# Optimization experiments

Measured on AMD Instinct MI355X. Metric: run time of the kernel, lower is better.

Reference implementation:

```python
import jax, jax.numpy as jnp
import numpy as np

N_NODES = 30000
N_EDGES = 480000
NODE_DIM = 16
NUM_RADIAL = 8
NUM_ELEMENTS = 120
R_MAX = 5.0
NUM_BLOCKS = 2
N_PATHS = 5  # h0*sh0->0e, h0*sh1->1o, h0*sh2->2e, h1.sh1->0e, h2.sh2->0e


def _sh_basis(u):
    # real spherical harmonics up to l=2, component normalization, on unit vectors u [E,3]
    x, y, z = u[:, 0], u[:, 1], u[:, 2]
    s15 = jnp.sqrt(jnp.asarray(15.0, u.dtype))
    s5 = jnp.sqrt(jnp.asarray(5.0, u.dtype))
    sh1 = jnp.sqrt(jnp.asarray(3.0, u.dtype)) * u                      # [E,3]
    sh2 = jnp.stack([s15 * x * y, s15 * y * z,
                     0.5 * s5 * (3.0 * z * z - 1.0),
                     s15 * x * z, 0.5 * s15 * (x * x - y * y)], -1)    # [E,5]
    return sh1, sh2


def _energy(pos, emb, W_init, Wr, br, W_out, W_read, W1, b1, W2, b2, z, edge_index):
    N = pos.shape[0]
    row, col = edge_index[0], edge_index[1]
    edge_vec = pos[row] - pos[col]                                     # [E,3] gather
    r = jnp.sqrt(jnp.sum(edge_vec * edge_vec, -1) + 1e-12)             # [E]
    n = jnp.arange(1, NUM_RADIAL + 1, dtype=pos.dtype)
    # Bessel radial basis: sqrt(2/rc) * sin(n*pi*r/rc)/r
    radial = jnp.sqrt(2.0 / R_MAX) * jnp.sin(n[None, :] * jnp.pi * r[:, None] / R_MAX) / r[:, None]  # [E,R]
    u = edge_vec / r[:, None]
    sh1, sh2 = _sh_basis(u)

    # initial projection: embedding scalars -> 0e channels; l=1,l=2 start at zero
    h0 = emb[z] @ W_init                                               # [N,C]
    h1 = jnp.zeros((N, NODE_DIM, 3), pos.dtype)
    h2 = jnp.zeros((N, NODE_DIM, 5), pos.dtype)

    for b in range(NUM_BLOCKS):
        w = (radial @ Wr[b] + br[b]).reshape(-1, N_PATHS, NODE_DIM)    # [E,P,C] radial path weights
        h0c, h1c, h2c = h0[col], h1[col], h2[col]
        # scalar messages: h0*sh0 + <h1,sh1> + <h2,sh2>
        m0 = (w[:, 0] * h0c
              + w[:, 3] * jnp.einsum('ecm,em->ec', h1c, sh1)
              + w[:, 4] * jnp.einsum('ecm,em->ec', h2c, sh2))          # [E,C]
        m1 = (w[:, 1] * h0c)[:, :, None] * sh1[:, None, :]             # [E,C,3]
        m2 = (w[:, 2] * h0c)[:, :, None] * sh2[:, None, :]             # [E,C,5]
        a0 = jax.ops.segment_sum(m0, row, num_segments=N)
        a1 = jax.ops.segment_sum(m1, row, num_segments=N)
        a2 = jax.ops.segment_sum(m2, row, num_segments=N)
        h0 = h0 + a0 @ W_out[b, 0]
        h1 = h1 + jnp.einsum('ncm,cd->ndm', a1, W_out[b, 1])
        h2 = h2 + jnp.einsum('ncm,cd->ndm', a2, W_out[b, 2])

    inv = h0 @ W_read                                                  # readout 0e part
    site = jax.nn.silu(inv @ W1 + b1) @ W2 + b2                        # [N,1]
    return jnp.sum(site)


def setup_inputs() -> dict:
    key = jax.random.key(0)
    ks = jax.random.split(key, 12)
    C, R = NODE_DIM, NUM_RADIAL
    s = 1.0 / np.sqrt(C)
    return {
        'pos': jax.random.normal(ks[0], (N_NODES, 3), jnp.float32) * 3.0,
        'z': jax.random.randint(ks[1], (N_NODES,), 0, NUM_ELEMENTS),
        'edge_index': jax.random.randint(ks[2], (2, N_EDGES), 0, N_NODES),
        'emb': jax.random.normal(ks[3], (NUM_ELEMENTS, C), jnp.float32),
        'W_init': jax.random.normal(ks[4], (C, C), jnp.float32) * s,
        'Wr': jax.random.normal(ks[5], (NUM_BLOCKS, R, N_PATHS * C), jnp.float32) / np.sqrt(R),
        'br': jnp.zeros((NUM_BLOCKS, N_PATHS * C), jnp.float32),
        'W_out': jax.random.normal(ks[6], (NUM_BLOCKS, 3, C, C), jnp.float32) * s,
        'W_read': jax.random.normal(ks[7], (C, C), jnp.float32) * s,
        'W1': jax.random.normal(ks[8], (C, C), jnp.float32) * s,
        'b1': jnp.zeros((C,), jnp.float32),
        'W2': jax.random.normal(ks[9], (C, 1), jnp.float32) * s,
        'b2': jnp.zeros((1,), jnp.float32),
    }


def reference(pos, z, edge_index, emb, W_init, Wr, br, W_out, W_read, W1, b1, W2, b2):
    e_fn = lambda p: _energy(p, emb, W_init, Wr, br, W_out, W_read, W1, b1, W2, b2, z, edge_index)
    total, dE_dpos = jax.value_and_grad(e_fn)(pos)
    energy = jnp.reshape(total, (1, 1))
    forces = -dE_dpos
    return energy, forces
```

## Files before the change

kernel.cpp:

```cpp
#include <hip/hip_runtime.h>
#include <math.h>

#ifndef M_PI
#define M_PI 3.14159265358979323846
#endif

static inline int cdiv(int a, int b){ return (a + b - 1) / b; }

#define SQRT3f  1.7320508075688772f
#define SQRT5f  2.23606797749979f
#define SQRT15f 3.872983346207417f
#define KRADf   0.6324555320336759f
#define PI5f    0.6283185307179586f
#define KPI5f   (KRADf * PI5f)


__device__ __forceinline__ float grp16_sum(float v){
  v += __shfl_xor(v, 1, 64);
  v += __shfl_xor(v, 2, 64);
  v += __shfl_xor(v, 4, 64);
  v += __shfl_xor(v, 8, 64);
  return v;
}
__device__ __forceinline__ float xgrp_sum(float v){
  v += __shfl_xor(v, 16, 64);
  v += __shfl_xor(v, 32, 64);
  return v;
}

__device__ __forceinline__ void sh_from_u(float ux, float uy, float uz,
                                          float* sh1, float* sh2)
{
  sh1[0] = SQRT3f*ux; sh1[1] = SQRT3f*uy; sh1[2] = SQRT3f*uz;
  sh2[0] = SQRT15f*ux*uy;
  sh2[1] = SQRT15f*uy*uz;
  sh2[2] = 0.5f*SQRT5f*(3.f*uz*uz - 1.f);
  sh2[3] = SQRT15f*ux*uz;
  sh2[4] = 0.5f*SQRT15f*(ux*ux - uy*uy);
}


__global__ void k_hist(const int* __restrict__ ei, int E,
                       int* __restrict__ deg_row, int* __restrict__ deg_col)
{
  int e = blockIdx.x * blockDim.x + threadIdx.x;
  if (e >= E) return;
  atomicAdd(&deg_row[ei[e]], 1);
  atomicAdd(&deg_col[ei[E + e]], 1);
}

__global__ void k_alloc(const int* __restrict__ deg_row, const int* __restrict__ deg_col,
                        int* __restrict__ start_row, int* __restrict__ cur_row,
                        int* __restrict__ start_col, int* __restrict__ cur_col,
                        int* __restrict__ cursors, int N)
{
  int idx = blockIdx.x * blockDim.x + threadIdx.x;
  int lane = threadIdx.x & 63;
  #pragma unroll
  for (int which = 0; which < 2; which++) {
    const int* deg = which ? deg_col : deg_row;
    int* start = which ? start_col : start_row;
    int* cur   = which ? cur_col   : cur_row;
    int v = (idx < N) ? deg[idx] : 0;
    int incl = v;
    #pragma unroll
    for (int d = 1; d < 64; d <<= 1) {
      int y = __shfl_up(incl, d, 64);
      if (lane >= d) incl += y;
    }
    int wtot = __shfl(incl, 63, 64);
    int base = 0;
    if (lane == 63) base = atomicAdd(&cursors[which], wtot);
    base = __shfl(base, 63, 64);
    if (idx < N) { int st = base + incl - v; start[idx] = st; cur[idx] = st; }
  }
}

__global__ void k_scatter_geom(const float* __restrict__ pos, const int* __restrict__ ei, int E,
                               int* __restrict__ cur_row, int* __restrict__ cur_col,
                               float4* __restrict__ uR, float2* __restrict__ scR,
                               float4* __restrict__ uC, float2* __restrict__ scC,
                               int* __restrict__ colR, int* __restrict__ cposR,
                               int* __restrict__ rowC, int* __restrict__ rposC)
{
  int e = blockIdx.x * blockDim.x + threadIdx.x;
  if (e >= E) return;
  int row = ei[e], col = ei[E + e];
  int pr = atomicAdd(&cur_row[row], 1);
  int pc = atomicAdd(&cur_col[col], 1);
  colR[pr] = col; cposR[pr] = pc;
  rowC[pc] = row; rposC[pc] = pr;

  float px = pos[row*3+0] - pos[col*3+0];
  float py = pos[row*3+1] - pos[col*3+1];
  float pz = pos[row*3+2] - pos[col*3+2];
  float r2 = px*px + py*py + pz*pz + 1e-12f;
  float r = sqrtf(r2);
  float inv_r = 1.0f / r;
  float ux = px*inv_r, uy = py*inv_r, uz = pz*inv_r;
  float s1, c1;
  sincosf(r * PI5f, &s1, &c1);
  float4 u4 = make_float4(ux, uy, uz, inv_r);
  float2 sc = make_float2(s1, c1);
  uR[pr] = u4; scR[pr] = sc;
  uC[pc] = u4; scC[pc] = sc;
}

__global__ void k_node_init(const float* __restrict__ emb, const int* __restrict__ z,
                            const float* __restrict__ W_init, float* __restrict__ h0, int N)
{
  __shared__ float sW[256];
  if (threadIdx.x < 256) sW[threadIdx.x] = W_init[threadIdx.x];
  __syncthreads();
  int n = blockIdx.x * blockDim.x + threadIdx.x;
  if (n >= N) return;
  const float* e = emb + z[n]*16;
  float ev[16];
  #pragma unroll
  for (int k = 0; k < 16; k++) ev[k] = e[k];
  #pragma unroll
  for (int c = 0; c < 16; c++) {
    float s = 0.f;
    #pragma unroll
    for (int k = 0; k < 16; k++) s += ev[k] * sW[k*16+c];
    h0[n*16+c] = s;
  }
}

__global__ void k_fwd_b0(const float* __restrict__ Wr, const float* __restrict__ br,
                         const float* __restrict__ h0_in,
                         const float4* __restrict__ uR, const float2* __restrict__ scR,
                         const int* __restrict__ colR,
                         const int* __restrict__ start_row, const int* __restrict__ deg_row,
                         float* __restrict__ a0, float* __restrict__ a1, float* __restrict__ a2,
                         int N)
{
  int wid = (blockIdx.x * blockDim.x + threadIdx.x) >> 6;
  int nw  = (gridDim.x * blockDim.x) >> 6;
  int lane = threadIdx.x & 63;
  int g = lane >> 4, c = lane & 15;
  float wr0[8], wr1[8], wr2[8];
  #pragma unroll
  for (int k = 0; k < 8; k++) {
    wr0[k] = Wr[k*80 + c];
    wr1[k] = Wr[k*80 + 16 + c];
    wr2[k] = Wr[k*80 + 32 + c];
  }
  float b0v = br[c], b1v = br[16 + c], b2v = br[32 + c];

  for (int n = wid; n < N; n += nw) {
    float acc0 = 0.f, acc1[3] = {0.f,0.f,0.f}, acc2[5] = {0.f,0.f,0.f,0.f,0.f};

    int i0 = start_row[n] + g, i1 = start_row[n] + deg_row[n];
    float4 Un = {0,0,0,0}; float2 SCn = {0,0};
    float h0n = 0.f;
    if (i0 < i1) {
      Un = uR[i0]; SCn = scR[i0];
      h0n = h0_in[colR[i0]*16 + c];
    }
    for (int i = i0; i < i1; i += 4) {
      float4 U = Un; float2 SC = SCn;
      float h0c = h0n;
      if (i+4 < i1) {
        Un = uR[i+4]; SCn = scR[i+4];
        h0n = h0_in[colR[i+4]*16 + c];
      }
      float Ki = KRADf * U.w;
      float tc = 2.f * SC.y;
      float sprev = 0.f, s = SC.x;
      float w0 = b0v, w1 = b1v, w2 = b2v;
      #pragma unroll
      for (int k = 0; k < 8; k++) {
        float rad = Ki * s;
        w0 += rad*wr0[k]; w1 += rad*wr1[k]; w2 += rad*wr2[k];
        float sn = tc*s - sprev; sprev = s; s = sn;
      }
      float sh1[3], sh2[5];
      sh_from_u(U.x, U.y, U.z, sh1, sh2);
      acc0 += w0*h0c;
      float wh1 = w1*h0c, wh2 = w2*h0c;
      #pragma unroll
      for (int m = 0; m < 3; m++) acc1[m] += wh1*sh1[m];
      #pragma unroll
      for (int m = 0; m < 5; m++) acc2[m] += wh2*sh2[m];
    }
    acc0 = xgrp_sum(acc0);
    #pragma unroll
    for (int m = 0; m < 3; m++) acc1[m] = xgrp_sum(acc1[m]);
    #pragma unroll
    for (int m = 0; m < 5; m++) acc2[m] = xgrp_sum(acc2[m]);
    if (g == 0) {
      a0[n*16 + c] = acc0;
      #pragma unroll
      for (int m = 0; m < 3; m++) a1[n*48 + c*3 + m] = acc1[m];
      #pragma unroll
      for (int m = 0; m < 5; m++) a2[n*80 + c*5 + m] = acc2[m];
    }
  }
}

__global__ void k_fwd_b1(const float* __restrict__ Wr, const float* __restrict__ br,
                         const float* __restrict__ h0_in, const float* __restrict__ h1_in,
                         const float* __restrict__ h2_in,
                         const float4* __restrict__ uR, const float2* __restrict__ scR,
                         const int* __restrict__ colR,
                         const int* __restrict__ start_row, const int* __restrict__ deg_row,
                         float* __restrict__ a0, int N)
{
  int wid = (blockIdx.x * blockDim.x + threadIdx.x) >> 6;
  int nw  = (gridDim.x * blockDim.x) >> 6;
  int lane = threadIdx.x & 63;
  int g = lane >> 4, c = lane & 15;
  float wr0[8], wr3[8], wr4[8];
  #pragma unroll
  for (int k = 0; k < 8; k++) {
    wr0[k] = Wr[k*80 + c];
    wr3[k] = Wr[k*80 + 48 + c];
    wr4[k] = Wr[k*80 + 64 + c];
  }
  float b0v = br[c], b3v = br[48 + c], b4v = br[64 + c];

  for (int n = wid; n < N; n += nw) {
    float acc0 = 0.f;
    int i0 = start_row[n] + g, i1 = start_row[n] + deg_row[n];
    float4 Un = {0,0,0,0}; float2 SCn = {0,0};
    float h0n = 0.f, h1n[3] = {0,0,0}, h2n[5] = {0,0,0,0,0};
    if (i0 < i1) {
      int col = colR[i0];
      Un = uR[i0]; SCn = scR[i0];
      h0n = h0_in[col*16 + c];
      #pragma unroll
      for (int m = 0; m < 3; m++) h1n[m] = h1_in[col*48 + c*3 + m];
      #pragma unroll
      for (int m = 0; m < 5; m++) h2n[m] = h2_in[col*80 + c*5 + m];
    }
    for (int i = i0; i < i1; i += 4) {
      float4 U = Un; float2 SC = SCn;
      float h0c = h0n;
      float h1c[3], h2c[5];
      #pragma unroll
      for (int m = 0; m < 3; m++) h1c[m] = h1n[m];
      #pragma unroll
      for (int m = 0; m < 5; m++) h2c[m] = h2n[m];
      if (i+4 < i1) {
        int col = colR[i+4];
        Un = uR[i+4]; SCn = scR[i+4];
        h0n = h0_in[col*16 + c];
        #pragma unroll
        for (int m = 0; m < 3; m++) h1n[m] = h1_in[col*48 + c*3 + m];
        #pragma unroll
        for (int m = 0; m < 5; m++) h2n[m] = h2_in[col*80 + c*5 + m];
      }
      float Ki = KRADf * U.w;
      float tc = 2.f * SC.y;
      float sprev = 0.f, s = SC.x;
      float w0 = b0v, w3 = b3v, w4 = b4v;
      #pragma unroll
      for (int k = 0; k < 8; k++) {
        float rad = Ki * s;
        w0 += rad*wr0[k]; w3 += rad*wr3[k]; w4 += rad*wr4[k];
        float sn = tc*s - sprev; sprev = s; s = sn;
      }
      float sh1[3], sh2[5];
      sh_from_u(U.x, U.y, U.z, sh1, sh2);
      float S1 = 0.f, S2 = 0.f;
      #pragma unroll
      for (int m = 0; m < 3; m++) S1 += h1c[m]*sh1[m];
      #pragma unroll
      for (int m = 0; m < 5; m++) S2 += h2c[m]*sh2[m];
      acc0 += w0*h0c + w3*S1 + w4*S2;
    }
    acc0 = xgrp_sum(acc0);
    if (g == 0) a0[n*16 + c] = acc0;
  }
}

__global__ void k_node_update(const float* __restrict__ h0_in,
                              const float* __restrict__ a0, const float* __restrict__ a1,
                              const float* __restrict__ a2,
                              const float* __restrict__ U,
                              float* __restrict__ h0_out, float* __restrict__ h1_out,
                              float* __restrict__ h2_out, int N)
{
  int idx = blockIdx.x * blockDim.x + threadIdx.x;
  int n = idx >> 4, d = idx & 15;
  if (n >= N) return;
  const float* U0 = U;
  const float* U1 = U + 256;
  const float* U2 = U + 512;
  float s = h0_in[n*16 + d];
  #pragma unroll
  for (int c = 0; c < 16; c++) s += a0[n*16 + c] * U0[c*16 + d];
  h0_out[n*16 + d] = s;
  float v1[3] = {0.f, 0.f, 0.f};
  #pragma unroll
  for (int c = 0; c < 16; c++) {
    float u = U1[c*16 + d];
    #pragma unroll
    for (int m = 0; m < 3; m++) v1[m] += a1[n*48 + c*3 + m] * u;
  }
  #pragma unroll
  for (int m = 0; m < 3; m++) h1_out[n*48 + d*3 + m] = v1[m];
  float v2[5] = {0.f, 0.f, 0.f, 0.f, 0.f};
  #pragma unroll
  for (int c = 0; c < 16; c++) {
    float u = U2[c*16 + d];
    #pragma unroll
    for (int m = 0; m < 5; m++) v2[m] += a2[n*80 + c*5 + m] * u;
  }
  #pragma unroll
  for (int m = 0; m < 5; m++) h2_out[n*80 + d*5 + m] = v2[m];
}

__global__ void __launch_bounds__(256, 1)
k_readout_bwd(const float* __restrict__ h0s1, const float* __restrict__ a0in,
              const float* __restrict__ W_read,
              const float* __restrict__ W1, const float* __restrict__ b1,
              const float* __restrict__ W2, const float* __restrict__ b2,
              const float* __restrict__ U0b1,
              float* __restrict__ g0, float* __restrict__ ga0,
              float* __restrict__ partials, int N)
{
  __shared__ float sWr[256], sW1[256], sU[256], sb1[16], sW2[16], sb2;
  __shared__ float swave[4];
  {
    int t = threadIdx.x;
    if (t < 256) { sWr[t] = W_read[t]; sW1[t] = W1[t]; sU[t] = U0b1[t]; }
    if (t < 16)  { sb1[t] = b1[t]; sW2[t] = W2[t]; }
    if (t == 0)  sb2 = b2[0];
  }
  __syncthreads();
  int n = blockIdx.x * blockDim.x + threadIdx.x;
  float site = 0.f;
  if (n < N) {
    float h[16], av[16], inv[16], dt[16], g0v[16];
    #pragma unroll
    for (int d = 0; d < 16; d++) av[d] = a0in[n*16 + d];
    #pragma unroll
    for (int d = 0; d < 16; d++) {
      float s = h0s1[n*16 + d];
      #pragma unroll
      for (int cc = 0; cc < 16; cc++) s += av[cc] * sU[cc*16 + d];
      h[d] = s;
    }
    #pragma unroll
    for (int j = 0; j < 16; j++) {
      float s = 0.f;
      #pragma unroll
      for (int d = 0; d < 16; d++) s += h[d] * sWr[d*16 + j];
      inv[j] = s;
    }
    site = sb2;
    #pragma unroll
    for (int c = 0; c < 16; c++) {
      float t = sb1[c];
      #pragma unroll
      for (int j = 0; j < 16; j++) t += inv[j] * sW1[j*16 + c];
      float sg = 1.f / (1.f + expf(-t));
      float w2v = sW2[c];
      site += t * sg * w2v;
      dt[c] = w2v * sg * (1.f + t * (1.f - sg));
    }
    float dinv[16];
    #pragma unroll
    for (int j = 0; j < 16; j++) {
      float s = 0.f;
      #pragma unroll
      for (int c = 0; c < 16; c++) s += dt[c] * sW1[j*16 + c];
      dinv[j] = s;
    }
    #pragma unroll
    for (int d = 0; d < 16; d++) {
      float s = 0.f;
      #pragma unroll
      for (int j = 0; j < 16; j++) s += dinv[j] * sWr[d*16 + j];
      g0v[d] = s;
      g0[n*16 + d] = s;
    }
    #pragma unroll
    for (int c = 0; c < 16; c++) {
      float s = 0.f;
      #pragma unroll
      for (int d = 0; d < 16; d++) s += g0v[d] * sU[c*16 + d];
      ga0[n*16 + c] = s;
    }
  }
  #pragma unroll
  for (int off = 32; off; off >>= 1) site += __shfl_down(site, off, 64);
  int wave = threadIdx.x >> 6;
  if ((threadIdx.x & 63) == 0) swave[wave] = site;
  __syncthreads();
  if (threadIdx.x == 0)
    partials[blockIdx.x] = swave[0] + swave[1] + swave[2] + swave[3];
}

__global__ void k_energy(const float* __restrict__ partials, int nb,
                         float* __restrict__ energy)
{
  int t = threadIdx.x;
  float s = 0.f;
  for (int i = t; i < nb; i += 128) s += partials[i];
  #pragma unroll
  for (int off = 32; off; off >>= 1) s += __shfl_down(s, off, 64);
  __shared__ float sw[2];
  if ((t & 63) == 0) sw[t >> 6] = s;
  __syncthreads();
  if (t == 0) energy[0] = sw[0] + sw[1];
}

__global__ void k_ga(const float* __restrict__ g0, const float* __restrict__ g1,
                     const float* __restrict__ g2, const float* __restrict__ U,
                     float* __restrict__ ga0, float* __restrict__ ga1, float* __restrict__ ga2,
                     int N)
{
  int idx = blockIdx.x * blockDim.x + threadIdx.x;
  int n = idx >> 4, c = idx & 15;
  if (n >= N) return;
  const float* U0 = U;
  const float* U1 = U + 256;
  const float* U2 = U + 512;
  float s = 0.f;
  #pragma unroll
  for (int d = 0; d < 16; d++) s += g0[n*16 + d] * U0[c*16 + d];
  ga0[n*16 + c] = s;
  float v1[3] = {0.f, 0.f, 0.f};
  #pragma unroll
  for (int d = 0; d < 16; d++) {
    float u = U1[c*16 + d];
    #pragma unroll
    for (int m = 0; m < 3; m++) v1[m] += g1[n*48 + d*3 + m] * u;
  }
  #pragma unroll
  for (int m = 0; m < 3; m++) ga1[n*48 + c*3 + m] = v1[m];
  float v2[5] = {0.f, 0.f, 0.f, 0.f, 0.f};
  #pragma unroll
  for (int d = 0; d < 16; d++) {
    float u = U2[c*16 + d];
    #pragma unroll
    for (int m = 0; m < 5; m++) v2[m] += g2[n*80 + d*5 + m] * u;
  }
  #pragma unroll
  for (int m = 0; m < 5; m++) ga2[n*80 + c*5 + m] = v2[m];
}

__global__ void k_bwd_b1_col(const float* __restrict__ Wr, const float* __restrict__ br,
                             const float* __restrict__ h0_in, const float* __restrict__ h1_in,
                             const float* __restrict__ h2_in,
                             const float* __restrict__ ga0,
                             const float4* __restrict__ uC, const float2* __restrict__ scC,
                             const int* __restrict__ rowC,
                             const int* __restrict__ start_col, const int* __restrict__ deg_col,
                             float* __restrict__ g0, float* __restrict__ g1, float* __restrict__ g2,
                             float* __restrict__ dv_col, int N)
{
  int wid = (blockIdx.x * blockDim.x + threadIdx.x) >> 6;
  int nw  = (gridDim.x * blockDim.x) >> 6;
  int lane = threadIdx.x & 63;
  int g = lane >> 4, c = lane & 15;
  float wr0[8], wr3[8], wr4[8];
  #pragma unroll
  for (int k = 0; k < 8; k++) {
    wr0[k] = Wr[k*80 + c];
    wr3[k] = Wr[k*80 + 48 + c];
    wr4[k] = Wr[k*80 + 64 + c];
  }
  float b0v = br[c], b3v = br[48 + c], b4v = br[64 + c];

  for (int n = wid; n < N; n += nw) {
    float h0c = h0_in[n*16 + c];
    float h1c[3], h2c[5];
    #pragma unroll
    for (int m = 0; m < 3; m++) h1c[m] = h1_in[n*48 + c*3 + m];
    #pragma unroll
    for (int m = 0; m < 5; m++) h2c[m] = h2_in[n*80 + c*5 + m];

    float accg0 = 0.f, accg1[3] = {0.f,0.f,0.f}, accg2[5] = {0.f,0.f,0.f,0.f,0.f};

    int i0 = start_col[n] + g, i1 = start_col[n] + deg_col[n];
    float4 Un = {0,0,0,0}; float2 SCn = {0,0};
    float dm0n = 0.f;
    if (i0 < i1) {
      Un = uC[i0]; SCn = scC[i0];
      dm0n = ga0[rowC[i0]*16 + c];
    }
    for (int i = i0; i < i1; i += 4) {
      float4 U = Un; float2 SC = SCn;
      float dm0 = dm0n;
      if (i+4 < i1) {
        Un = uC[i+4]; SCn = scC[i+4];
        dm0n = ga0[rowC[i+4]*16 + c];
      }
      float ux = U.x, uy = U.y, uz = U.z, inv_r = U.w;
      float sh1[3], sh2[5];
      sh_from_u(ux, uy, uz, sh1, sh2);

      float S1 = 0.f, S2 = 0.f;
      #pragma unroll
      for (int m = 0; m < 3; m++) S1 += h1c[m]*sh1[m];
      #pragma unroll
      for (int m = 0; m < 5; m++) S2 += h2c[m]*sh2[m];

      float dw0 = dm0 * h0c;
      float dw3 = dm0 * S1;
      float dw4 = dm0 * S2;

      float Ki = KRADf * inv_r;
      float tc = 2.f * SC.y;
      float sprev = 0.f, s = SC.x, cprev = 1.f, cc = SC.y;
      float w0 = b0v, w3 = b3v, w4 = b4v;
      float P = 0.f, Q = 0.f;
      #pragma unroll
      for (int k = 0; k < 8; k++) {
        float rad = Ki * s;
        w0 += rad*wr0[k]; w3 += rad*wr3[k]; w4 += rad*wr4[k];
        float t = dw0*wr0[k] + dw3*wr3[k] + dw4*wr4[k];
        P = fmaf(t*cc, (float)(k+1), P);
        Q = fmaf(t, rad, Q);
        float sn = tc*s - sprev; sprev = s; s = sn;
        float cn = tc*cc - cprev; cprev = cc; cc = cn;
      }

      float t3 = dm0 * w3, t4 = dm0 * w4;
      accg0 += dm0 * w0;
      #pragma unroll
      for (int m = 0; m < 3; m++) accg1[m] += t3 * sh1[m];
      #pragma unroll
      for (int m = 0; m < 5; m++) accg2[m] += t4 * sh2[m];

      float q1x = t3*h1c[0], q1y = t3*h1c[1], q1z = t3*h1c[2];
      float q0 = t4*h2c[0], q1 = t4*h2c[1], q2 = t4*h2c[2], q3 = t4*h2c[3], q4 = t4*h2c[4];
      float gr = (KPI5f*P - Q) * inv_r;
      float gux = SQRT3f*q1x + SQRT15f*(uy*q0 + uz*q3 + ux*q4);
      float guy = SQRT3f*q1y + SQRT15f*(ux*q0 + uz*q1 - uy*q4);
      float guz = SQRT3f*q1z + SQRT15f*uy*q1 + 3.f*SQRT5f*uz*q2 + SQRT15f*ux*q3;

      gr  = grp16_sum(gr);
      gux = grp16_sum(gux);
      guy = grp16_sum(guy);
      guz = grp16_sum(guz);

      if (c == 0) {
        float gdotu = gux*ux + guy*uy + guz*uz;
        dv_col[i*3+0] = gr*ux + (gux - gdotu*ux)*inv_r;
        dv_col[i*3+1] = gr*uy + (guy - gdotu*uy)*inv_r;
        dv_col[i*3+2] = gr*uz + (guz - gdotu*uz)*inv_r;
      }
    }
    accg0 = xgrp_sum(accg0);
    #pragma unroll
    for (int m = 0; m < 3; m++) accg1[m] = xgrp_sum(accg1[m]);
    #pragma unroll
    for (int m = 0; m < 5; m++) accg2[m] = xgrp_sum(accg2[m]);
    if (g == 0) {
      g0[n*16 + c] += accg0;
      #pragma unroll
      for (int m = 0; m < 3; m++) g1[n*48 + c*3 + m] = accg1[m];
      #pragma unroll
      for (int m = 0; m < 5; m++) g2[n*80 + c*5 + m] = accg2[m];
    }
  }
}

__global__ void k_bwd_b0_row(const float* __restrict__ Wr, const float* __restrict__ br,
                             const float* __restrict__ h0_in,
                             const float* __restrict__ ga0, const float* __restrict__ ga1,
                             const float* __restrict__ ga2,
                             const float4* __restrict__ uR, const float2* __restrict__ scR,
                             const int* __restrict__ colR,
                             const int* __restrict__ start_row, const int* __restrict__ deg_row,
                             float* __restrict__ dv_row, int N)
{
  int wid = (blockIdx.x * blockDim.x + threadIdx.x) >> 6;
  int nw  = (gridDim.x * blockDim.x) >> 6;
  int lane = threadIdx.x & 63;
  int g = lane >> 4, c = lane & 15;
  float wr0[8], wr1[8], wr2[8];
  #pragma unroll
  for (int k = 0; k < 8; k++) {
    wr0[k] = Wr[k*80 + c];
    wr1[k] = Wr[k*80 + 16 + c];
    wr2[k] = Wr[k*80 + 32 + c];
  }
  float b1v = br[16 + c], b2v = br[32 + c];

  for (int n = wid; n < N; n += nw) {
    float dm0 = ga0[n*16 + c];
    float dm1[3], dm2[5];
    #pragma unroll
    for (int m = 0; m < 3; m++) dm1[m] = ga1[n*48 + c*3 + m];
    #pragma unroll
    for (int m = 0; m < 5; m++) dm2[m] = ga2[n*80 + c*5 + m];

    int i0 = start_row[n] + g, i1 = start_row[n] + deg_row[n];
    float4 Un = {0,0,0,0}; float2 SCn = {0,0};
    float h0n = 0.f;
    if (i0 < i1) {
      Un = uR[i0]; SCn = scR[i0];
      h0n = h0_in[colR[i0]*16 + c];
    }
    for (int i = i0; i < i1; i += 4) {
      float4 U = Un; float2 SC = SCn;
      float h0c = h0n;
      if (i+4 < i1) {
        Un = uR[i+4]; SCn = scR[i+4];
        h0n = h0_in[colR[i+4]*16 + c];
      }
      float ux = U.x, uy = U.y, uz = U.z, inv_r = U.w;
      float sh1[3], sh2[5];
      sh_from_u(ux, uy, uz, sh1, sh2);

      float T1 = 0.f, T2 = 0.f;
      #pragma unroll
      for (int m = 0; m < 3; m++) T1 += dm1[m]*sh1[m];
      #pragma unroll
      for (int m = 0; m < 5; m++) T2 += dm2[m]*sh2[m];

      float dw0 = dm0 * h0c;
      float dw1 = h0c * T1;
      float dw2 = h0c * T2;

      float Ki = KRADf * inv_r;
      float tc = 2.f * SC.y;
      float sprev = 0.f, s = SC.x, cprev = 1.f, cc = SC.y;
      float w1 = b1v, w2v = b2v;
      float P = 0.f, Q = 0.f;
      #pragma unroll
      for (int k = 0; k < 8; k++) {
        float rad = Ki * s;
        w1 += rad*wr1[k]; w2v += rad*wr2[k];
        float t = dw0*wr0[k] + dw1*wr1[k] + dw2*wr2[k];
        P = fmaf(t*cc, (float)(k+1), P);
        Q = fmaf(t, rad, Q);
        float sn = tc*s - sprev; sprev = s; s = sn;
        float cn = tc*cc - cprev; cprev = cc; cc = cn;
      }

      float w1h = w1*h0c, w2h = w2v*h0c;
      float q1x = dm1[0]*w1h, q1y = dm1[1]*w1h, q1z = dm1[2]*w1h;
      float q0 = dm2[0]*w2h, q1 = dm2[1]*w2h, q2 = dm2[2]*w2h, q3 = dm2[3]*w2h, q4 = dm2[4]*w2h;

      float gr = (KPI5f*P - Q) * inv_r;
      float gux = SQRT3f*q1x + SQRT15f*(uy*q0 + uz*q3 + ux*q4);
      float guy = SQRT3f*q1y + SQRT15f*(ux*q0 + uz*q1 - uy*q4);
      float guz = SQRT3f*q1z + SQRT15f*uy*q1 + 3.f*SQRT5f*uz*q2 + SQRT15f*ux*q3;

      gr  = grp16_sum(gr);
      gux = grp16_sum(gux);
      guy = grp16_sum(guy);
      guz = grp16_sum(guz);

      if (c == 0) {
        float gdotu = gux*ux + guy*uy + guz*uz;
        dv_row[i*3+0] = gr*ux + (gux - gdotu*ux)*inv_r;
        dv_row[i*3+1] = gr*uy + (guy - gdotu*uy)*inv_r;
        dv_row[i*3+2] = gr*uz + (guz - gdotu*uz)*inv_r;
      }
    }
  }
}

__global__ void k_force(const int* __restrict__ start_row, const int* __restrict__ deg_row,
                        const int* __restrict__ cposR,
                        const int* __restrict__ start_col, const int* __restrict__ deg_col,
                        const int* __restrict__ rposC,
                        const float* __restrict__ dv_col, const float* __restrict__ dv_row,
                        float* __restrict__ force, int N)
{
  int idx = blockIdx.x * blockDim.x + threadIdx.x;
  int n = idx >> 4, l = idx & 15;
  if (n >= N) return;
  float fx = 0.f, fy = 0.f, fz = 0.f;
  int c0 = start_col[n], c1 = c0 + deg_col[n];
  for (int i = c0 + l; i < c1; i += 16) {
    int rp = rposC[i];
    fx += dv_col[i*3+0] + dv_row[rp*3+0];
    fy += dv_col[i*3+1] + dv_row[rp*3+1];
    fz += dv_col[i*3+2] + dv_row[rp*3+2];
  }
  int r0 = start_row[n], r1 = r0 + deg_row[n];
  for (int i = r0 + l; i < r1; i += 16) {
    int cp = cposR[i];
    fx -= dv_row[i*3+0] + dv_col[cp*3+0];
    fy -= dv_row[i*3+1] + dv_col[cp*3+1];
    fz -= dv_row[i*3+2] + dv_col[cp*3+2];
  }
  fx = grp16_sum(fx); fy = grp16_sum(fy); fz = grp16_sum(fz);
  if (l == 0) {
    force[n*3+0] = fx; force[n*3+1] = fy; force[n*3+2] = fz;
  }
}

extern "C" void kernel_launch(void* const* d_in, const int* in_sizes, int n_in,
                              void* d_out, int out_size, void* d_ws, size_t ws_size,
                              hipStream_t stream)
{
  const float* pos    = (const float*)d_in[0];
  const int*   z      = (const int*)  d_in[1];
  const int*   ei     = (const int*)  d_in[2];
  const float* emb    = (const float*)d_in[3];
  const float* W_init = (const float*)d_in[4];
  const float* Wr     = (const float*)d_in[5];
  const float* br     = (const float*)d_in[6];
  const float* W_out  = (const float*)d_in[7];
  const float* W_read = (const float*)d_in[8];
  const float* W1     = (const float*)d_in[9];
  const float* b1     = (const float*)d_in[10];
  const float* W2     = (const float*)d_in[11];
  const float* b2     = (const float*)d_in[12];

  const int N = in_sizes[0] / 3;
  const int E = in_sizes[2] / 2;

  const int BLK = 256;
  const int NB_READOUT = cdiv(N, BLK);
  const int PBLK = (N < 8192) ? cdiv(N, 4) : 2048;

  float* f = (float*)d_ws;
  float4* uR  = (float4*)f; f += (size_t)E*4;
  float4* uC  = (float4*)f; f += (size_t)E*4;
  float2* scR = (float2*)f; f += (size_t)E*2;
  float2* scC = (float2*)f; f += (size_t)E*2;
  float* h0_s0 = f; f += (size_t)N*16;
  float* h0_s1 = f; f += (size_t)N*16;
  float* h1_s1 = f; f += (size_t)N*48;
  float* h2_s1 = f; f += (size_t)N*80;
  float* a0    = f; f += (size_t)N*16;
  float* a1    = f; f += (size_t)N*48;
  float* a2    = f; f += (size_t)N*80;
  float* ga0b1 = f; f += (size_t)N*16;
  float* g0    = f; f += (size_t)N*16;
  float* g1    = f; f += (size_t)N*48;
  float* g2    = f; f += (size_t)N*80;
  float* dv_c  = f; f += (size_t)E*3;
  float* dv_r  = f; f += (size_t)E*3;
  float* partials = f; f += (size_t)NB_READOUT;
  int* ip = (int*)f;
  int* cursors   = ip; ip += 2;
  int* deg_row   = ip; ip += N;
  int* deg_col   = ip; ip += N;
  int* start_row = ip; ip += N;
  int* start_col = ip; ip += N;
  int* cur_row   = ip; ip += N;
  int* cur_col   = ip; ip += N;
  int* colR      = ip; ip += E;
  int* cposR     = ip; ip += E;
  int* rowC      = ip; ip += E;
  int* rposC     = ip; ip += E;

  float* out    = (float*)d_out;
  float* energy = out;
  float* force  = out + 1;

  (void)hipMemsetAsync(cursors, 0, (size_t)(2 + 2*N) * sizeof(int), stream);

  k_hist<<<cdiv(E, BLK), BLK, 0, stream>>>(ei, E, deg_row, deg_col);
  k_alloc<<<cdiv(N, BLK), BLK, 0, stream>>>(deg_row, deg_col, start_row, cur_row,
                                            start_col, cur_col, cursors, N);
  k_scatter_geom<<<cdiv(E, BLK), BLK, 0, stream>>>(pos, ei, E, cur_row, cur_col,
                                                   uR, scR, uC, scC,
                                                   colR, cposR, rowC, rposC);

  k_node_init<<<cdiv(N, BLK), BLK, 0, stream>>>(emb, z, W_init, h0_s0, N);

  k_fwd_b0<<<PBLK, BLK, 0, stream>>>(Wr, br, h0_s0, uR, scR, colR,
                                     start_row, deg_row, a0, a1, a2, N);
  k_node_update<<<cdiv(N*16, BLK), BLK, 0, stream>>>(h0_s0, a0, a1, a2,
                                                     W_out, h0_s1, h1_s1, h2_s1, N);

  k_fwd_b1<<<PBLK, BLK, 0, stream>>>(Wr + 640, br + 80,
                                     h0_s1, h1_s1, h2_s1, uR, scR, colR,
                                     start_row, deg_row, a0, N);

  k_readout_bwd<<<NB_READOUT, BLK, 0, stream>>>(h0_s1, a0, W_read, W1, b1, W2, b2,
                                                W_out + 768, g0, ga0b1, partials, N);
  k_energy<<<1, 128, 0, stream>>>(partials, NB_READOUT, energy);

  k_bwd_b1_col<<<PBLK, BLK, 0, stream>>>(Wr + 640, br + 80,
                                         h0_s1, h1_s1, h2_s1, ga0b1,
                                         uC, scC, rowC, start_col, deg_col,
                                         g0, g1, g2, dv_c, N);

  k_ga<<<cdiv(N*16, BLK), BLK, 0, stream>>>(g0, g1, g2, W_out, a0, a1, a2, N);
  k_bwd_b0_row<<<PBLK, BLK, 0, stream>>>(Wr, br, h0_s0,
                                         a0, a1, a2, uR, scR, colR,
                                         start_row, deg_row, dv_r, N);

  k_force<<<cdiv(N*16, BLK), BLK, 0, stream>>>(start_row, deg_row, cposR,
                                               start_col, deg_col, rposC,
                                               dv_c, dv_r, force, N);
}
```

Baseline: 473.4 us.

## Scatter edge force contributions via atomics and fold SH constants into node data

The per-edge dv buffers and the separate force-gather kernel are removed. The two backward edge kernels now atomically add each edge's displacement gradient directly into the force array, which is zeroed up front. The cposR/rposC permutation arrays and their writes are dropped. Spherical-harmonic normalization constants move out of the per-edge loops into per-node pre/post scaling, and __launch_bounds__(256,8) is added to the edge kernels. The cost is six float atomics per edge, which may contend on high-degree nodes, and force summation order becomes nondeterministic.

```diff
diff --git a/kernel.cpp b/kernel.cpp
--- a/kernel.cpp
+++ b/kernel.cpp
@@ -13,6 +13,8 @@
 #define KRADf   0.6324555320336759f
 #define PI5f    0.6283185307179586f
 #define KPI5f   (KRADf * PI5f)
+#define CSH2f   (0.5f*SQRT5f)
+#define CSH4f   (0.5f*SQRT15f)
 
 
 __device__ __forceinline__ float grp16_sum(float v){
@@ -28,15 +30,14 @@
   return v;
 }
 
-__device__ __forceinline__ void sh_from_u(float ux, float uy, float uz,
-                                          float* sh1, float* sh2)
-{
-  sh1[0] = SQRT3f*ux; sh1[1] = SQRT3f*uy; sh1[2] = SQRT3f*uz;
-  sh2[0] = SQRT15f*ux*uy;
-  sh2[1] = SQRT15f*uy*uz;
-  sh2[2] = 0.5f*SQRT5f*(3.f*uz*uz - 1.f);
-  sh2[3] = SQRT15f*ux*uz;
-  sh2[4] = 0.5f*SQRT15f*(ux*ux - uy*uy);
+__device__ __forceinline__ void base2_from_u(float ux, float uy, float uz, float* b2)
+{
+  float z2 = uz*uz, x2 = ux*ux, y2 = uy*uy;
+  b2[0] = ux*uy;
+  b2[1] = uy*uz;
+  b2[2] = fmaf(z2, 3.f, -1.f);
+  b2[3] = ux*uz;
+  b2[4] = x2 - y2;
 }
 
 
@@ -80,16 +81,15 @@
                                int* __restrict__ cur_row, int* __restrict__ cur_col,
                                float4* __restrict__ uR, float2* __restrict__ scR,
                                float4* __restrict__ uC, float2* __restrict__ scC,
-                               int* __restrict__ colR, int* __restrict__ cposR,
-                               int* __restrict__ rowC, int* __restrict__ rposC)
+                               int* __restrict__ colR, int* __restrict__ rowC)
 {
   int e = blockIdx.x * blockDim.x + threadIdx.x;
   if (e >= E) return;
   int row = ei[e], col = ei[E + e];
   int pr = atomicAdd(&cur_row[row], 1);
   int pc = atomicAdd(&cur_col[col], 1);
-  colR[pr] = col; cposR[pr] = pc;
-  rowC[pc] = row; rposC[pc] = pr;
+  colR[pr] = col;
+  rowC[pc] = row;
 
   float px = pos[row*3+0] - pos[col*3+0];
   float py = pos[row*3+1] - pos[col*3+1];
@@ -127,13 +127,14 @@
   }
 }
 
-__global__ void k_fwd_b0(const float* __restrict__ Wr, const float* __restrict__ br,
-                         const float* __restrict__ h0_in,
-                         const float4* __restrict__ uR, const float2* __restrict__ scR,
-                         const int* __restrict__ colR,
-                         const int* __restrict__ start_row, const int* __restrict__ deg_row,
-                         float* __restrict__ a0, float* __restrict__ a1, float* __restrict__ a2,
-                         int N)
+__global__ void __launch_bounds__(256, 8)
+k_fwd_b0(const float* __restrict__ Wr, const float* __restrict__ br,
+         const float* __restrict__ h0_in,
+         const float4* __restrict__ uR, const float2* __restrict__ scR,
+         const int* __restrict__ colR,
+         const int* __restrict__ start_row, const int* __restrict__ deg_row,
+         float* __restrict__ a0, float* __restrict__ a1, float* __restrict__ a2,
+         int N)
 {
   int wid = (blockIdx.x * blockDim.x + threadIdx.x) >> 6;
   int nw  = (gridDim.x * blockDim.x) >> 6;
@@ -175,14 +176,13 @@
         w0 += rad*wr0[k]; w1 += rad*wr1[k]; w2 += rad*wr2[k];
         float sn = tc*s - sprev; sprev = s; s = sn;
       }
-      float sh1[3], sh2[5];
-      sh_from_u(U.x, U.y, U.z, sh1, sh2);
+      float b2[5];
+      base2_from_u(U.x, U.y, U.z, b2);
       acc0 += w0*h0c;
       float wh1 = w1*h0c, wh2 = w2*h0c;
-      #pragma unroll
-      for (int m = 0; m < 3; m++) acc1[m] += wh1*sh1[m];
-      #pragma unroll
-      for (int m = 0; m < 5; m++) acc2[m] += wh2*sh2[m];
+      acc1[0] += wh1*U.x; acc1[1] += wh1*U.y; acc1[2] += wh1*U.z;
+      #pragma unroll
+      for (int m = 0; m < 5; m++) acc2[m] += wh2*b2[m];
     }
     acc0 = xgrp_sum(acc0);
     #pragma unroll
@@ -191,21 +191,26 @@
     for (int m = 0; m < 5; m++) acc2[m] = xgrp_sum(acc2[m]);
     if (g == 0) {
       a0[n*16 + c] = acc0;
-      #pragma unroll
-      for (int m = 0; m < 3; m++) a1[n*48 + c*3 + m] = acc1[m];
-      #pragma unroll
-      for (int m = 0; m < 5; m++) a2[n*80 + c*5 + m] = acc2[m];
-    }
-  }
-}
-
-__global__ void k_fwd_b1(const float* __restrict__ Wr, const float* __restrict__ br,
-                         const float* __restrict__ h0_in, const float* __restrict__ h1_in,
-                         const float* __restrict__ h2_in,
-                         const float4* __restrict__ uR, const float2* __restrict__ scR,
-                         const int* __restrict__ colR,
-                         const int* __restrict__ start_row, const int* __restrict__ deg_row,
-                         float* __restrict__ a0, int N)
+      a1[n*48 + c*3 + 0] = SQRT3f*acc1[0];
+      a1[n*48 + c*3 + 1] = SQRT3f*acc1[1];
+      a1[n*48 + c*3 + 2] = SQRT3f*acc1[2];
+      a2[n*80 + c*5 + 0] = SQRT15f*acc2[0];
+      a2[n*80 + c*5 + 1] = SQRT15f*acc2[1];
+      a2[n*80 + c*5 + 2] = CSH2f  *acc2[2];
+      a2[n*80 + c*5 + 3] = SQRT15f*acc2[3];
+      a2[n*80 + c*5 + 4] = CSH4f  *acc2[4];
+    }
+  }
+}
+
+__global__ void __launch_bounds__(256, 8)
+k_fwd_b1(const float* __restrict__ Wr, const float* __restrict__ br,
+         const float* __restrict__ h0_in, const float* __restrict__ h1_in,
+         const float* __restrict__ h2_in,
+         const float4* __restrict__ uR, const float2* __restrict__ scR,
+         const int* __restrict__ colR,
+         const int* __restrict__ start_row, const int* __restrict__ deg_row,
+         float* __restrict__ a0, int N)
 {
   int wid = (blockIdx.x * blockDim.x + threadIdx.x) >> 6;
   int nw  = (gridDim.x * blockDim.x) >> 6;
@@ -215,10 +220,10 @@
   #pragma unroll
   for (int k = 0; k < 8; k++) {
     wr0[k] = Wr[k*80 + c];
-    wr3[k] = Wr[k*80 + 48 + c];
+    wr3[k] = SQRT3f*Wr[k*80 + 48 + c];
     wr4[k] = Wr[k*80 + 64 + c];
   }
-  float b0v = br[c], b3v = br[48 + c], b4v = br[64 + c];
+  float b0v = br[c], b3v = SQRT3f*br[48 + c], b4v = br[64 + c];
 
   for (int n = wid; n < N; n += nw) {
     float acc0 = 0.f;
@@ -261,13 +266,12 @@
         w0 += rad*wr0[k]; w3 += rad*wr3[k]; w4 += rad*wr4[k];
         float sn = tc*s - sprev; sprev = s; s = sn;
       }
-      float sh1[3], sh2[5];
-      sh_from_u(U.x, U.y, U.z, sh1, sh2);
-      float S1 = 0.f, S2 = 0.f;
-      #pragma unroll
-      for (int m = 0; m < 3; m++) S1 += h1c[m]*sh1[m];
-      #pragma unroll
-      for (int m = 0; m < 5; m++) S2 += h2c[m]*sh2[m];
+      float b2[5];
+      base2_from_u(U.x, U.y, U.z, b2);
+      float S1 = h1c[0]*U.x + h1c[1]*U.y + h1c[2]*U.z;
+      float A  = h2c[0]*b2[0] + h2c[1]*b2[1] + h2c[3]*b2[3];
+      float B  = CSH2f*(h2c[2]*b2[2]) + CSH4f*(h2c[4]*b2[4]);
+      float S2 = fmaf(SQRT15f, A, B);
       acc0 += w0*h0c + w3*S1 + w4*S2;
     }
     acc0 = xgrp_sum(acc0);
@@ -443,15 +447,16 @@
   for (int m = 0; m < 5; m++) ga2[n*80 + c*5 + m] = v2[m];
 }
 
-__global__ void k_bwd_b1_col(const float* __restrict__ Wr, const float* __restrict__ br,
-                             const float* __restrict__ h0_in, const float* __restrict__ h1_in,
-                             const float* __restrict__ h2_in,
-                             const float* __restrict__ ga0,
-                             const float4* __restrict__ uC, const float2* __restrict__ scC,
-                             const int* __restrict__ rowC,
-                             const int* __restrict__ start_col, const int* __restrict__ deg_col,
-                             float* __restrict__ g0, float* __restrict__ g1, float* __restrict__ g2,
-                             float* __restrict__ dv_col, int N)
+__global__ void __launch_bounds__(256, 8)
+k_bwd_b1_col(const float* __restrict__ Wr, const float* __restrict__ br,
+             const float* __restrict__ h0_in, const float* __restrict__ h1_in,
+             const float* __restrict__ h2_in,
+             const float* __restrict__ ga0,
+             const float4* __restrict__ uC, const float2* __restrict__ scC,
+             const int* __restrict__ rowC,
+             const int* __restrict__ start_col, const int* __restrict__ deg_col,
+             float* __restrict__ g0, float* __restrict__ g1, float* __restrict__ g2,
+             float* __restrict__ force, int N)
 {
   int wid = (blockIdx.x * blockDim.x + threadIdx.x) >> 6;
   int nw  = (gridDim.x * blockDim.x) >> 6;
@@ -468,44 +473,47 @@
 
   for (int n = wid; n < N; n += nw) {
     float h0c = h0_in[n*16 + c];
-    float h1c[3], h2c[5];
-    #pragma unroll
-    for (int m = 0; m < 3; m++) h1c[m] = h1_in[n*48 + c*3 + m];
-    #pragma unroll
-    for (int m = 0; m < 5; m++) h2c[m] = h2_in[n*80 + c*5 + m];
+    float h1s[3], h2s[5];
+    #pragma unroll
+    for (int m = 0; m < 3; m++) h1s[m] = SQRT3f * h1_in[n*48 + c*3 + m];
+    h2s[0] = SQRT15f * h2_in[n*80 + c*5 + 0];
+    h2s[1] = SQRT15f * h2_in[n*80 + c*5 + 1];
+    h2s[2] = CSH2f   * h2_in[n*80 + c*5 + 2];
+    h2s[3] = SQRT15f * h2_in[n*80 + c*5 + 3];
+    h2s[4] = CSH4f   * h2_in[n*80 + c*5 + 4];
 
     float accg0 = 0.f, accg1[3] = {0.f,0.f,0.f}, accg2[5] = {0.f,0.f,0.f,0.f,0.f};
 
     int i0 = start_col[n] + g, i1 = start_col[n] + deg_col[n];
     float4 Un = {0,0,0,0}; float2 SCn = {0,0};
-    float dm0n = 0.f;
+    float dm0n = 0.f; int rn = 0;
     if (i0 < i1) {
+      rn = rowC[i0];
       Un = uC[i0]; SCn = scC[i0];
-      dm0n = ga0[rowC[i0]*16 + c];
+      dm0n = ga0[rn*16 + c];
     }
     for (int i = i0; i < i1; i += 4) {
       float4 U = Un; float2 SC = SCn;
-      float dm0 = dm0n;
+      float dm0 = dm0n; int rcur = rn;
       if (i+4 < i1) {
+        rn = rowC[i+4];
         Un = uC[i+4]; SCn = scC[i+4];
-        dm0n = ga0[rowC[i+4]*16 + c];
+        dm0n = ga0[rn*16 + c];
       }
       float ux = U.x, uy = U.y, uz = U.z, inv_r = U.w;
-      float sh1[3], sh2[5];
-      sh_from_u(ux, uy, uz, sh1, sh2);
-
-      float S1 = 0.f, S2 = 0.f;
-      #pragma unroll
-      for (int m = 0; m < 3; m++) S1 += h1c[m]*sh1[m];
-      #pragma unroll
-      for (int m = 0; m < 5; m++) S2 += h2c[m]*sh2[m];
+      float b2[5];
+      base2_from_u(ux, uy, uz, b2);
+
+      float S1 = h1s[0]*ux + h1s[1]*uy + h1s[2]*uz;
+      float S2 = h2s[0]*b2[0] + h2s[1]*b2[1] + h2s[2]*b2[2]
+               + h2s[3]*b2[3] + h2s[4]*b2[4];
 
       float dw0 = dm0 * h0c;
       float dw3 = dm0 * S1;
       float dw4 = dm0 * S2;
 
       float Ki = KRADf * inv_r;
-      float tc = 2.f * SC.y;
+      float tcv = 2.f * SC.y;
       float sprev = 0.f, s = SC.x, cprev = 1.f, cc = SC.y;
       float w0 = b0v, w3 = b3v, w4 = b4v;
       float P = 0.f, Q = 0.f;
@@ -516,23 +524,24 @@
         float t = dw0*wr0[k] + dw3*wr3[k] + dw4*wr4[k];
         P = fmaf(t*cc, (float)(k+1), P);
         Q = fmaf(t, rad, Q);
-        float sn = tc*s - sprev; sprev = s; s = sn;
-        float cn = tc*cc - cprev; cprev = cc; cc = cn;
+        float sn = tcv*s - sprev; sprev = s; s = sn;
+        float cn = tcv*cc - cprev; cprev = cc; cc = cn;
       }
 
       float t3 = dm0 * w3, t4 = dm0 * w4;
       accg0 += dm0 * w0;
-      #pragma unroll
-      for (int m = 0; m < 3; m++) accg1[m] += t3 * sh1[m];
-      #pragma unroll
-      for (int m = 0; m < 5; m++) accg2[m] += t4 * sh2[m];
-
-      float q1x = t3*h1c[0], q1y = t3*h1c[1], q1z = t3*h1c[2];
-      float q0 = t4*h2c[0], q1 = t4*h2c[1], q2 = t4*h2c[2], q3 = t4*h2c[3], q4 = t4*h2c[4];
+      accg1[0] += t3*ux; accg1[1] += t3*uy; accg1[2] += t3*uz;
+      #pragma unroll
+      for (int m = 0; m < 5; m++) accg2[m] += t4*b2[m];
+
+      float q1x = t3*h1s[0], q1y = t3*h1s[1], q1z = t3*h1s[2];
+      float q0 = t4*h2s[0], q1 = t4*h2s[1], q2 = t4*h2s[2], q3 = t4*h2s[3], q4 = t4*h2s[4];
+      float q4d = q4 + q4;
+      float q2h = 6.f*q2;
       float gr = (KPI5f*P - Q) * inv_r;
-      float gux = SQRT3f*q1x + SQRT15f*(uy*q0 + uz*q3 + ux*q4);
-      float guy = SQRT3f*q1y + SQRT15f*(ux*q0 + uz*q1 - uy*q4);
-      float guz = SQRT3f*q1z + SQRT15f*uy*q1 + 3.f*SQRT5f*uz*q2 + SQRT15f*ux*q3;
+      float gux = q1x + uy*q0 + uz*q3 + ux*q4d;
+      float guy = q1y + ux*q0 + uz*q1 - uy*q4d;
+      float guz = q1z + uy*q1 + uz*q2h + ux*q3;
 
       gr  = grp16_sum(gr);
       gux = grp16_sum(gux);
@@ -541,9 +550,15 @@
 
       if (c == 0) {
         float gdotu = gux*ux + guy*uy + guz*uz;
-        dv_col[i*3+0] = gr*ux + (gux - gdotu*ux)*inv_r;
-        dv_col[i*3+1] = gr*uy + (guy - gdotu*uy)*inv_r;
-        dv_col[i*3+2] = gr*uz + (guz - gdotu*uz)*inv_r;
+        float dvx = gr*ux + (gux - gdotu*ux)*inv_r;
+        float dvy = gr*uy + (guy - gdotu*uy)*inv_r;
+        float dvz = gr*uz + (guz - gdotu*uz)*inv_r;
+        atomicAdd(&force[n*3+0],  dvx);
+        atomicAdd(&force[n*3+1],  dvy);
+        atomicAdd(&force[n*3+2],  dvz);
+        atomicAdd(&force[rcur*3+0], -dvx);
+        atomicAdd(&force[rcur*3+1], -dvy);
+        atomicAdd(&force[rcur*3+2], -dvz);
       }
     }
     accg0 = xgrp_sum(accg0);
@@ -553,22 +568,27 @@
     for (int m = 0; m < 5; m++) accg2[m] = xgrp_sum(accg2[m]);
     if (g == 0) {
       g0[n*16 + c] += accg0;
-      #pragma unroll
-      for (int m = 0; m < 3; m++) g1[n*48 + c*3 + m] = accg1[m];
-      #pragma unroll
-      for (int m = 0; m < 5; m++) g2[n*80 + c*5 + m] = accg2[m];
-    }
-  }
-}
-
-__global__ void k_bwd_b0_row(const float* __restrict__ Wr, const float* __restrict__ br,
-                             const float* __restrict__ h0_in,
-                             const float* __restrict__ ga0, const float* __restrict__ ga1,
-                             const float* __restrict__ ga2,
-                             const float4* __restrict__ uR, const float2* __restrict__ scR,
-                             const int* __restrict__ colR,
-                             const int* __restrict__ start_row, const int* __restrict__ deg_row,
-                             float* __restrict__ dv_row, int N)
+      g1[n*48 + c*3 + 0] = SQRT3f*accg1[0];
+      g1[n*48 + c*3 + 1] = SQRT3f*accg1[1];
+      g1[n*48 + c*3 + 2] = SQRT3f*accg1[2];
+      g2[n*80 + c*5 + 0] = SQRT15f*accg2[0];
+      g2[n*80 + c*5 + 1] = SQRT15f*accg2[1];
+      g2[n*80 + c*5 + 2] = CSH2f  *accg2[2];
+      g2[n*80 + c*5 + 3] = SQRT15f*accg2[3];
+      g2[n*80 + c*5 + 4] = CSH4f  *accg2[4];
+    }
+  }
+}
+
+__global__ void __launch_bounds__(256, 8)
+k_bwd_b0_row(const float* __restrict__ Wr, const float* __restrict__ br,
+             const float* __restrict__ h0_in,
+             const float* __restrict__ ga0, const float* __restrict__ ga1,
+             const float* __restrict__ ga2,
+             const float4* __restrict__ uR, const float2* __restrict__ scR,
+             const int* __restrict__ colR,
+             const int* __restrict__ start_row, const int* __restrict__ deg_row,
+             float* __restrict__ force, int N)
 {
   int wid = (blockIdx.x * blockDim.x + threadIdx.x) >> 6;
   int nw  = (gridDim.x * blockDim.x) >> 6;
@@ -585,42 +605,45 @@
 
   for (int n = wid; n < N; n += nw) {
     float dm0 = ga0[n*16 + c];
-    float dm1[3], dm2[5];
-    #pragma unroll
-    for (int m = 0; m < 3; m++) dm1[m] = ga1[n*48 + c*3 + m];
-    #pragma unroll
-    for (int m = 0; m < 5; m++) dm2[m] = ga2[n*80 + c*5 + m];
+    float dm1s[3], dm2s[5];
+    #pragma unroll
+    for (int m = 0; m < 3; m++) dm1s[m] = SQRT3f * ga1[n*48 + c*3 + m];
+    dm2s[0] = SQRT15f * ga2[n*80 + c*5 + 0];
+    dm2s[1] = SQRT15f * ga2[n*80 + c*5 + 1];
+    dm2s[2] = CSH2f   * ga2[n*80 + c*5 + 2];
+    dm2s[3] = SQRT15f * ga2[n*80 + c*5 + 3];
+    dm2s[4] = CSH4f   * ga2[n*80 + c*5 + 4];
 
     int i0 = start_row[n] + g, i1 = start_row[n] + deg_row[n];
     float4 Un = {0,0,0,0}; float2 SCn = {0,0};
-    float h0n = 0.f;
+    float h0n = 0.f; int cn = 0;
     if (i0 < i1) {
+      cn = colR[i0];
       Un = uR[i0]; SCn = scR[i0];
-      h0n = h0_in[colR[i0]*16 + c];
+      h0n = h0_in[cn*16 + c];
     }
     for (int i = i0; i < i1; i += 4) {
       float4 U = Un; float2 SC = SCn;
-      float h0c = h0n;
+      float h0c = h0n; int ccur = cn;
       if (i+4 < i1) {
+        cn = colR[i+4];
         Un = uR[i+4]; SCn = scR[i+4];
-        h0n = h0_in[colR[i+4]*16 + c];
+        h0n = h0_in[cn*16 + c];
       }
       float ux = U.x, uy = U.y, uz = U.z, inv_r = U.w;
-      float sh1[3], sh2[5];
-      sh_from_u(ux, uy, uz, sh1, sh2);
-
-      float T1 = 0.f, T2 = 0.f;
-      #pragma unroll
-      for (int m = 0; m < 3; m++) T1 += dm1[m]*sh1[m];
-      #pragma unroll
-      for (int m = 0; m < 5; m++) T2 += dm2[m]*sh2[m];
+      float b2[5];
+      base2_from_u(ux, uy, uz, b2);
+
+      float T1 = dm1s[0]*ux + dm1s[1]*uy + dm1s[2]*uz;
+      float T2 = dm2s[0]*b2[0] + dm2s[1]*b2[1] + dm2s[2]*b2[2]
+               + dm2s[3]*b2[3] + dm2s[4]*b2[4];
 
       float dw0 = dm0 * h0c;
       float dw1 = h0c * T1;
       float dw2 = h0c * T2;
 
       float Ki = KRADf * inv_r;
-      float tc = 2.f * SC.y;
+      float tcv = 2.f * SC.y;
       float sprev = 0.f, s = SC.x, cprev = 1.f, cc = SC.y;
       float w1 = b1v, w2v = b2v;
       float P = 0.f, Q = 0.f;
@@ -631,18 +654,19 @@
         float t = dw0*wr0[k] + dw1*wr1[k] + dw2*wr2[k];
         P = fmaf(t*cc, (float)(k+1), P);
         Q = fmaf(t, rad, Q);
-        float sn = tc*s - sprev; sprev = s; s = sn;
-        float cn = tc*cc - cprev; cprev = cc; cc = cn;
+        float sn = tcv*s - sprev; sprev = s; s = sn;
+        float cn2 = tcv*cc - cprev; cprev = cc; cc = cn2;
       }
 
       float w1h = w1*h0c, w2h = w2v*h0c;
-      float q1x = dm1[0]*w1h, q1y = dm1[1]*w1h, q1z = dm1[2]*w1h;
-      float q0 = dm2[0]*w2h, q1 = dm2[1]*w2h, q2 = dm2[2]*w2h, q3 = dm2[3]*w2h, q4 = dm2[4]*w2h;
-
+      float q1x = dm1s[0]*w1h, q1y = dm1s[1]*w1h, q1z = dm1s[2]*w1h;
+      float q0 = dm2s[0]*w2h, q1 = dm2s[1]*w2h, q2 = dm2s[2]*w2h, q3 = dm2s[3]*w2h, q4 = dm2s[4]*w2h;
+      float q4d = q4 + q4;
+      float q2h = 6.f*q2;
       float gr = (KPI5f*P - Q) * inv_r;
-      float gux = SQRT3f*q1x + SQRT15f*(uy*q0 + uz*q3 + ux*q4);
-      float guy = SQRT3f*q1y + SQRT15f*(ux*q0 + uz*q1 - uy*q4);
-      float guz = SQRT3f*q1z + SQRT15f*uy*q1 + 3.f*SQRT5f*uz*q2 + SQRT15f*ux*q3;
+      float gux = q1x + uy*q0 + uz*q3 + ux*q4d;
+      float guy = q1y + ux*q0 + uz*q1 - uy*q4d;
+      float guz = q1z + uy*q1 + uz*q2h + ux*q3;
 
       gr  = grp16_sum(gr);
       gux = grp16_sum(gux);
@@ -651,42 +675,17 @@
 
       if (c == 0) {
         float gdotu = gux*ux + guy*uy + guz*uz;
-        dv_row[i*3+0] = gr*ux + (gux - gdotu*ux)*inv_r;
-        dv_row[i*3+1] = gr*uy + (guy - gdotu*uy)*inv_r;
-        dv_row[i*3+2] = gr*uz + (guz - gdotu*uz)*inv_r;
-      }
-    }
-  }
-}
-
-__global__ void k_force(const int* __restrict__ start_row, const int* __restrict__ deg_row,
-                        const int* __restrict__ cposR,
-                        const int* __restrict__ start_col, const int* __restrict__ deg_col,
-                        const int* __restrict__ rposC,
-                        const float* __restrict__ dv_col, const float* __restrict__ dv_row,
-                        float* __restrict__ force, int N)
-{
-  int idx = blockIdx.x * blockDim.x + threadIdx.x;
-  int n = idx >> 4, l = idx & 15;
-  if (n >= N) return;
-  float fx = 0.f, fy = 0.f, fz = 0.f;
-  int c0 = start_col[n], c1 = c0 + deg_col[n];
-  for (int i = c0 + l; i < c1; i += 16) {
-    int rp = rposC[i];
-    fx += dv_col[i*3+0] + dv_row[rp*3+0];
-    fy += dv_col[i*3+1] + dv_row[rp*3+1];
-    fz += dv_col[i*3+2] + dv_row[rp*3+2];
-  }
-  int r0 = start_row[n], r1 = r0 + deg_row[n];
-  for (int i = r0 + l; i < r1; i += 16) {
-    int cp = cposR[i];
-    fx -= dv_row[i*3+0] + dv_col[cp*3+0];
-    fy -= dv_row[i*3+1] + dv_col[cp*3+1];
-    fz -= dv_row[i*3+2] + dv_col[cp*3+2];
-  }
-  fx = grp16_sum(fx); fy = grp16_sum(fy); fz = grp16_sum(fz);
-  if (l == 0) {
-    force[n*3+0] = fx; force[n*3+1] = fy; force[n*3+2] = fz;
+        float dvx = gr*ux + (gux - gdotu*ux)*inv_r;
+        float dvy = gr*uy + (guy - gdotu*uy)*inv_r;
+        float dvz = gr*uz + (guz - gdotu*uz)*inv_r;
+        atomicAdd(&force[ccur*3+0],  dvx);
+        atomicAdd(&force[ccur*3+1],  dvy);
+        atomicAdd(&force[ccur*3+2],  dvz);
+        atomicAdd(&force[n*3+0], -dvx);
+        atomicAdd(&force[n*3+1], -dvy);
+        atomicAdd(&force[n*3+2], -dvz);
+      }
+    }
   }
 }
 
@@ -731,8 +730,6 @@
   float* g0    = f; f += (size_t)N*16;
   float* g1    = f; f += (size_t)N*48;
   float* g2    = f; f += (size_t)N*80;
-  float* dv_c  = f; f += (size_t)E*3;
-  float* dv_r  = f; f += (size_t)E*3;
   float* partials = f; f += (size_t)NB_READOUT;
   int* ip = (int*)f;
   int* cursors   = ip; ip += 2;
@@ -743,22 +740,20 @@
   int* cur_row   = ip; ip += N;
   int* cur_col   = ip; ip += N;
   int* colR      = ip; ip += E;
-  int* cposR     = ip; ip += E;
   int* rowC      = ip; ip += E;
-  int* rposC     = ip; ip += E;
 
   float* out    = (float*)d_out;
   float* energy = out;
   float* force  = out + 1;
 
   (void)hipMemsetAsync(cursors, 0, (size_t)(2 + 2*N) * sizeof(int), stream);
+  (void)hipMemsetAsync(force, 0, (size_t)N * 3 * sizeof(float), stream);
 
   k_hist<<<cdiv(E, BLK), BLK, 0, stream>>>(ei, E, deg_row, deg_col);
   k_alloc<<<cdiv(N, BLK), BLK, 0, stream>>>(deg_row, deg_col, start_row, cur_row,
                                             start_col, cur_col, cursors, N);
   k_scatter_geom<<<cdiv(E, BLK), BLK, 0, stream>>>(pos, ei, E, cur_row, cur_col,
-                                                   uR, scR, uC, scC,
-                                                   colR, cposR, rowC, rposC);
+                                                   uR, scR, uC, scC, colR, rowC);
 
   k_node_init<<<cdiv(N, BLK), BLK, 0, stream>>>(emb, z, W_init, h0_s0, N);
 
@@ -778,14 +773,10 @@
   k_bwd_b1_col<<<PBLK, BLK, 0, stream>>>(Wr + 640, br + 80,
                                          h0_s1, h1_s1, h2_s1, ga0b1,
                                          uC, scC, rowC, start_col, deg_col,
-                                         g0, g1, g2, dv_c, N);
+                                         g0, g1, g2, force, N);
 
   k_ga<<<cdiv(N*16, BLK), BLK, 0, stream>>>(g0, g1, g2, W_out, a0, a1, a2, N);
   k_bwd_b0_row<<<PBLK, BLK, 0, stream>>>(Wr, br, h0_s0,
                                          a0, a1, a2, uR, scR, colR,
-                                         start_row, deg_row, dv_r, N);
-
-  k_force<<<cdiv(N*16, BLK), BLK, 0, stream>>>(start_row, deg_row, cposR,
-                                               start_col, deg_col, rposC,
-                                               dv_c, dv_r, force, N);
-}
+                                         start_row, deg_row, force, N);
+}
```

After: 1.070 ms. 2.26x slower.
